# Optimization experiments

Measured on AMD Instinct MI355X. Metric: run time of the kernel, lower is better.

## Reference

```python
import jax, jax.numpy as jnp
import numpy as np

NUM_HEADS = 8
EPS = 1e-12  # torch F.normalize eps


def setup_inputs() -> dict:
    key = jax.random.key(0)
    k1, k2, k3 = jax.random.split(key, 3)
    B, N, C = 8, 4096, 768
    x = jax.random.normal(k1, (B, N, C), dtype=jnp.float32)
    Wqkv = jax.random.normal(k2, (C, 3 * C), dtype=jnp.float32) * 0.02
    temperature = jnp.ones((NUM_HEADS, 1, 1), dtype=jnp.float32)
    Wproj = jax.random.normal(k3, (C, C), dtype=jnp.float32) * 0.02
    bproj = jnp.zeros((C,), dtype=jnp.float32)
    return {"x": x, "Wqkv": Wqkv, "temperature": temperature,
            "Wproj": Wproj, "bproj": bproj}


def _l2norm(t):
    # torch F.normalize(dim=-1): x / max(||x||, eps)
    n = jnp.sqrt(jnp.sum(t * t, axis=-1, keepdims=True))
    return t / jnp.maximum(n, EPS)


def reference(x, Wqkv, temperature, Wproj, bproj):
    B, N, C = x.shape
    H = NUM_HEADS
    Ch = C // H
    qkv = (x @ Wqkv).reshape(B, N, 3, H, Ch)
    qkv = qkv.transpose(2, 0, 3, 1, 4)           # (3, B, H, N, Ch)
    q, k, v = qkv[0], qkv[1], qkv[2]
    # transpose(-2,-1): attend over channels -> (B, H, Ch, N)
    q = jnp.swapaxes(q, -2, -1)
    k = jnp.swapaxes(k, -2, -1)
    v = jnp.swapaxes(v, -2, -1)
    q = _l2norm(q)
    k = _l2norm(k)
    # (B, H, Ch, Ch) channel-attention scores, scaled by learned temperature
    attn = jnp.einsum('bhcn,bhdn->bhcd', q, k) * temperature
    attn = jax.nn.softmax(attn, axis=-1)
    out = jnp.einsum('bhcd,bhdn->bhcn', attn, v)  # (B, H, Ch, N)
    out = out.transpose(0, 3, 1, 2).reshape(B, N, C)
    return out @ Wproj + bproj
```

## Files before the change

kernel.cpp:

```cpp
#include <hip/hip_runtime.h>
#include <cstdint>
#include <cstddef>

typedef unsigned short u16;
typedef short bf16x8 __attribute__((ext_vector_type(8)));
typedef unsigned short u16x4 __attribute__((ext_vector_type(4)));
typedef unsigned short u16x8 __attribute__((ext_vector_type(8)));
typedef float f32x4 __attribute__((ext_vector_type(4)));

#define EPSN 1e-12f

__device__ __forceinline__ u16 f2bf(float f) {
  uint32_t u = __builtin_bit_cast(uint32_t, f);
  u += 0x7FFFu + ((u >> 16) & 1u);
  return (u16)(u >> 16);
}
__device__ __forceinline__ float bf2f(u16 h) {
  uint32_t u = ((uint32_t)h) << 16;
  return __builtin_bit_cast(float, u);
}

__device__ __forceinline__ void gll16(const u16* g, u16* l) {
  __builtin_amdgcn_global_load_lds(
      (const __attribute__((address_space(1))) void*)g,
      (__attribute__((address_space(3))) void*)l, 16, 0, 0);
}

__global__ __launch_bounds__(256)
void k_cvtT(const float* __restrict__ x, u16* __restrict__ Xh,
            u16* __restrict__ XhT) {
  __shared__ u16 tr[64][68];
  const int tid = threadIdx.x;
  const int t0 = blockIdx.x * 64, k0 = blockIdx.y * 64, b = blockIdx.z;
  const size_t base = ((size_t)b * 4096 + t0) * 768 + k0;
#pragma unroll
  for (int p = 0; p < 4; p++) {
    const int r = (tid >> 4) + p * 16;
    const int c = (tid & 15) * 4;
    f32x4 v = *(const f32x4*)(x + base + (size_t)r * 768 + c);
    u16x4 o;
#pragma unroll
    for (int e = 0; e < 4; e++) o[e] = f2bf(v[e]);
    *(u16x4*)(Xh + base + (size_t)r * 768 + c) = o;
    tr[c + 0][r] = o[0];
    tr[c + 1][r] = o[1];
    tr[c + 2][r] = o[2];
    tr[c + 3][r] = o[3];
  }
  __syncthreads();
  const size_t tbase = ((size_t)b * 768 + k0) * 4096 + t0;
#pragma unroll
  for (int p = 0; p < 4; p++) {
    const int kk = (tid >> 4) + p * 16;
    const int ts = (tid & 15) * 4;
    u16x4 o;
#pragma unroll
    for (int e = 0; e < 4; e++) o[e] = tr[kk][ts + e];
    *(u16x4*)(XhT + tbase + (size_t)kk * 4096 + ts) = o;
  }
}

__global__ __launch_bounds__(256)
void k_wt(const float* __restrict__ W, u16* __restrict__ Wt, u16* __restrict__ Wvh) {
  __shared__ float tile[32][33];
  const int j0 = blockIdx.x * 32;
  const int k0 = blockIdx.y * 32;
  const int tx = threadIdx.x & 31;
  const int ty = threadIdx.x >> 5;
#pragma unroll
  for (int r = 0; r < 4; r++) {
    float v = W[(size_t)(k0 + ty + r * 8) * 2304 + j0 + tx];
    tile[ty + r * 8][tx] = v;
    if (j0 >= 1536)
      Wvh[(size_t)(k0 + ty + r * 8) * 768 + (j0 - 1536) + tx] = f2bf(v);
  }
  __syncthreads();
  if (j0 < 1536) {
#pragma unroll
    for (int r = 0; r < 4; r++)
      Wt[(size_t)(j0 + ty + r * 8) * 768 + k0 + tx] = f2bf(tile[tx][ty + r * 8]);
  }
}

template <int OUTF32B, int TRI>
__global__ __launch_bounds__(256, 3)
void k_gemm(const u16* __restrict__ A, const u16* __restrict__ Btp,
            void* __restrict__ Cp, const float* __restrict__ bias,
            int K, int lda, int ldb, int ldc,
            long aZ, long bZ, long cZ, int zK, long kss) {
  const int gx = gridDim.x, gy = gridDim.y;
  int f = blockIdx.x + gx * (blockIdx.y + gy * blockIdx.z);
  const int total = gx * gy * gridDim.z;
  const int q = total >> 3, rr = total & 7;
  const int xcd = f & 7, kk0 = f >> 3;
  f = (xcd < rr ? xcd * (q + 1) : rr * (q + 1) + (xcd - rr) * q) + kk0;
  const int bx = f % gx;
  const int tmp = f / gx;
  const int by = tmp % gy;
  const int bz = tmp / gy;

  int m0, n0;
  if constexpr (TRI) {
    const int ty = (bx >= 20) ? 5 : (bx >= 18) ? 4 : (bx >= 15) ? 3
                 : (bx >= 11) ? 2 : (bx >= 6) ? 1 : 0;
    const int txi = ty + (bx - (ty * 6 - (ty * (ty - 1)) / 2));
    m0 = ty * 128;
    n0 = txi * 128;
  } else {
    m0 = by * 128;
    n0 = bx * 128;
  }
  const int z = bz;
  const int bb = z / zK, ss = z % zK;
  const u16* Az = A + (long)bb * aZ + (long)ss * kss;
  const u16* Btz = Btp + (long)bb * bZ + (long)ss * kss;

  __shared__ u16 As[3 * 128 * 32];
  __shared__ u16 Bs[3 * 128 * 32];
  const int tid = threadIdx.x;
  const int lane = tid & 63;
  const int wid = tid >> 6;
  const int wr = wid >> 1, wc = wid & 1;
  const int fm = lane & 15, kg = lane >> 4;

  const int lr = lane >> 2;
  const int gk = (lane & 3) ^ ((lane >> 3) & 3);
  const u16* gA = Az + (size_t)(m0 + wid * 32 + lr) * lda + gk * 8;
  const u16* gB = Btz + (size_t)(n0 + wid * 32 + lr) * ldb + gk * 8;
  const size_t a16 = (size_t)16 * lda, b16 = (size_t)16 * ldb;
  u16* lA = As + wid * 1024;
  u16* lB = Bs + wid * 1024;
  const int kq = (kg ^ ((fm >> 1) & 3)) * 8;

  auto STAGE = [&](int slot, int ko) {
    u16* la = lA + slot * 4096;
    u16* lb = lB + slot * 4096;
    gll16(gA + ko, la);
    gll16(gA + ko + a16, la + 512);
    gll16(gB + ko, lb);
    gll16(gB + ko + b16, lb + 512);
  };

  const int nt = K >> 5;
  STAGE(0, 0);
  STAGE(1, 32);
  int sC = 0, sN = 1, sS = 2;

  f32x4 acc[4][4] = {};
  for (int t = 0; t < nt; ++t) {
    if (t + 2 < nt) {
      STAGE(sS, (t + 2) * 32);
      __builtin_amdgcn_sched_barrier(0);
      asm volatile("s_waitcnt vmcnt(8)" ::: "memory");
    } else if (t + 2 == nt) {
      asm volatile("s_waitcnt vmcnt(4)" ::: "memory");
    } else {
      asm volatile("s_waitcnt vmcnt(0)" ::: "memory");
    }
    __builtin_amdgcn_sched_barrier(0);
    __builtin_amdgcn_s_barrier();
    __builtin_amdgcn_sched_barrier(0);

    const u16* as_ = As + sC * 4096;
    const u16* bs_ = Bs + sC * 4096;
    bf16x8 af[4], bfr[4];
#pragma unroll
    for (int i = 0; i < 4; i++)
      af[i] = *(const bf16x8*)&as_[(wr * 64 + i * 16 + fm) * 32 + kq];
#pragma unroll
    for (int j = 0; j < 4; j++)
      bfr[j] = *(const bf16x8*)&bs_[(wc * 64 + j * 16 + fm) * 32 + kq];
    asm volatile("s_waitcnt lgkmcnt(0)" ::: "memory");
    __builtin_amdgcn_sched_barrier(0);
    __builtin_amdgcn_s_barrier();
    __builtin_amdgcn_sched_barrier(0);

#pragma unroll
    for (int i = 0; i < 4; i++)
#pragma unroll
      for (int j = 0; j < 4; j++)
        acc[i][j] = __builtin_amdgcn_mfma_f32_16x16x32_bf16(af[i], bfr[j], acc[i][j], 0, 0, 0);

    const int t2 = sC; sC = sN; sN = sS; sS = t2;
  }

  if constexpr (OUTF32B) {
    float* C = (float*)Cp + (long)z * cZ;
#pragma unroll
    for (int j = 0; j < 4; j++) {
      const int col = n0 + wc * 64 + j * 16 + fm;
      const float bj = bias[col];
#pragma unroll
      for (int i = 0; i < 4; i++) {
        const int r0 = m0 + wr * 64 + i * 16 + kg * 4;
#pragma unroll
        for (int r = 0; r < 4; r++)
          C[(size_t)(r0 + r) * ldc + col] = acc[i][j][r] + bj;
      }
    }
  } else {
    const int rb = TRI ? 0 : m0;
    const int cb = TRI ? 0 : n0;
    const int ld = TRI ? 128 : ldc;
    u16* C = (u16*)Cp + (long)z * cZ + (TRI ? (long)bx * 16384 : 0L);
#pragma unroll
    for (int j = 0; j < 4; j++) {
      const int col = cb + wc * 64 + j * 16 + fm;
#pragma unroll
      for (int i = 0; i < 4; i++) {
        const int r0 = rb + wr * 64 + i * 16 + kg * 4;
#pragma unroll
        for (int r = 0; r < 4; r++)
          C[(size_t)(r0 + r) * ld + col] = f2bf(acc[i][j][r]);
      }
    }
  }
}

__global__ __launch_bounds__(256)
void k_red(const u16* __restrict__ P, u16* __restrict__ O) {
  const int b = blockIdx.y;
  const int ti = blockIdx.x / 6, tj = blockIdx.x % 6;
  const bool mirror = ti > tj;
  const int a = mirror ? tj : ti;
  const int c2 = mirror ? ti : tj;
  const int src = a * 6 - (a * (a - 1)) / 2 + (c2 - a);
  __shared__ u16 lt[128 * 128];
  const int tid = threadIdx.x;
  const int r = tid >> 1;
  const int ch = (tid & 1) * 64;
  float acc[64] = {};
  for (int s = 0; s < 4; s++) {
    const u16* p = P + ((size_t)(b * 4 + s) * 344064 + (size_t)src * 16384);
    __syncthreads();
#pragma unroll
    for (int it = 0; it < 8; it++) {
      const int idx = (tid + it * 256) * 8;
      *(u16x8*)&lt[idx] = *(const u16x8*)(p + idx);
    }
    __syncthreads();
    if (!mirror) {
#pragma unroll
      for (int e = 0; e < 64; e++) acc[e] += bf2f(lt[r * 128 + ch + e]);
    } else {
#pragma unroll
      for (int e = 0; e < 64; e++) acc[e] += bf2f(lt[(ch + e) * 128 + r]);
    }
  }
  u16* o = O + (size_t)b * 589824 + (size_t)(ti * 128 + r) * 768 + tj * 128 + ch;
#pragma unroll
  for (int v8 = 0; v8 < 8; v8++) {
    u16x8 w;
#pragma unroll
    for (int e = 0; e < 8; e++) w[e] = f2bf(acc[v8 * 8 + e]);
    *(u16x8*)(o + v8 * 8) = w;
  }
}

__global__ __launch_bounds__(256)
void k_score(const u16* __restrict__ Tm, const u16* __restrict__ Wt,
             const float* __restrict__ temperature, float* __restrict__ Aattn) {
  const int h = blockIdx.x, b = blockIdx.y;
  const int bh = b * 8 + h;
  __shared__ u16 As[96 * 32];
  __shared__ u16 Bs[96 * 32];
  __shared__ u16 Dt2[96 * 32];
  __shared__ u16 Dwq[96 * 32];
  __shared__ float Gs[96 * 96];
  __shared__ float nqs[96], nks[96], invk[96];

  const int tid = threadIdx.x;
  const int lane = tid & 63;
  const int wid = tid >> 6;
  const int wr = wid >> 1, wc = wid & 1;
  const int fm = lane & 15, kg = lane >> 4;
  const int lr = lane >> 2;
  const int gkS = (lane & 3) ^ ((lane >> 3) & 3);
  const int gkL = (lane & 3);
  const int kq = (kg ^ ((fm >> 1) & 3)) * 8;

  const u16* baseT1 = Tm + (size_t)b * 1179648 + (size_t)(h * 96) * 768;
  const u16* baseT2 = baseT1 + (size_t)768 * 768;
  const u16* baseWq = Wt + (size_t)(h * 96) * 768;
  const u16* baseWk = baseWq + (size_t)768 * 768;

  const u16* gsrc;
  u16* ldst;
  int gblk = gkS;
  if (wid == 0) { gsrc = baseT1; ldst = As; }
  else if (wid == 1) { gsrc = baseWk; ldst = Bs; }
  else if (wid == 2) { gsrc = baseT2; ldst = Dt2; gblk = gkL; }
  else { gsrc = baseWq; ldst = Dwq; gblk = gkL; }

  f32x4 acc[3][3] = {};
  float nqa = 0.f, nka = 0.f;
  const int sw1 = (tid < 96) ? ((tid >> 1) & 3) : 0;
  const int sw2 = (tid >= 128 && tid < 224) ? (((tid - 128) >> 1) & 3) : 0;

  for (int k0 = 0; k0 < 768; k0 += 32) {
    __syncthreads();
#pragma unroll
    for (int c = 0; c < 6; c++) {
      gll16(gsrc + (size_t)(c * 16 + lr) * 768 + k0 + gblk * 8,
            ldst + c * 512);
    }
    __syncthreads();
    bf16x8 af[3], bfr[3];
#pragma unroll
    for (int i = 0; i < 3; i++)
      af[i] = *(const bf16x8*)&As[(wr * 48 + i * 16 + fm) * 32 + kq];
#pragma unroll
    for (int j = 0; j < 3; j++)
      bfr[j] = *(const bf16x8*)&Bs[(wc * 48 + j * 16 + fm) * 32 + kq];
#pragma unroll
    for (int i = 0; i < 3; i++)
#pragma unroll
      for (int j = 0; j < 3; j++)
        acc[i][j] = __builtin_amdgcn_mfma_f32_16x16x32_bf16(af[i], bfr[j], acc[i][j], 0, 0, 0);
    if (tid < 96) {
#pragma unroll
      for (int g = 0; g < 4; g++) {
        u16x8 av = *(const u16x8*)&As[tid * 32 + (g ^ sw1) * 8];
        u16x8 w = *(const u16x8*)&Dwq[tid * 32 + g * 8];
#pragma unroll
        for (int e = 0; e < 8; e++) nqa += bf2f(av[e]) * bf2f(w[e]);
      }
    } else if (tid >= 128 && tid < 224) {
      const int d = tid - 128;
#pragma unroll
      for (int g = 0; g < 4; g++) {
        u16x8 av = *(const u16x8*)&Bs[d * 32 + (g ^ sw2) * 8];
        u16x8 w = *(const u16x8*)&Dt2[d * 32 + g * 8];
#pragma unroll
        for (int e = 0; e < 8; e++) nka += bf2f(av[e]) * bf2f(w[e]);
      }
    }
  }

  if (tid < 96) nqs[tid] = nqa;
  if (tid >= 128 && tid < 224) nks[tid - 128] = nka;
#pragma unroll
  for (int i = 0; i < 3; i++)
#pragma unroll
    for (int j = 0; j < 3; j++)
#pragma unroll
      for (int r = 0; r < 4; r++)
        Gs[(wr * 48 + i * 16 + kg * 4 + r) * 96 + wc * 48 + j * 16 + fm] = acc[i][j][r];
  __syncthreads();
  if (tid < 96) invk[tid] = 1.0f / fmaxf(sqrtf(nks[tid]), EPSN);
  __syncthreads();
  if (tid < 96) {
    const int c = tid;
    const float iq = temperature[h] / fmaxf(sqrtf(nqs[c]), EPSN);
    float sv[96];
    float m = -1e30f;
#pragma unroll
    for (int d = 0; d < 96; d++) {
      float s = Gs[c * 96 + d] * iq * invk[d];
      sv[d] = s;
      m = fmaxf(m, s);
    }
    float sum = 0.f;
#pragma unroll
    for (int d = 0; d < 96; d++) {
      float e = __expf(sv[d] - m);
      sv[d] = e;
      sum += e;
    }
    const float inv = 1.0f / sum;
    float* dst = Aattn + (size_t)bh * 9216 + (size_t)c * 96;
#pragma unroll
    for (int d = 0; d < 96; d++) dst[d] = sv[d] * inv;
  }
}

__global__ __launch_bounds__(256)
void k_weff(const float* __restrict__ Aattn, const float* __restrict__ Wproj,
            u16* __restrict__ Weff) {
  const int jt = blockIdx.x, h = blockIdx.y, b = blockIdx.z;
  const int bh = b * 8 + h;
  __shared__ float As2[9216];
  const int tid = threadIdx.x;
  for (int idx = tid; idx < 9216; idx += 256)
    As2[idx] = Aattn[(size_t)bh * 9216 + idx];
  __syncthreads();
  const int jloc = tid & 127;
  const int half = tid >> 7;
  const int j = jt * 128 + jloc;
  float acc[48] = {};
  for (int c = 0; c < 96; c++) {
    const float w = Wproj[(size_t)(h * 96 + c) * 768 + j];
    const f32x4* ar = (const f32x4*)&As2[c * 96 + half * 48];
#pragma unroll
    for (int v4 = 0; v4 < 12; v4++) {
      f32x4 av = ar[v4];
      acc[v4 * 4 + 0] += w * av[0];
      acc[v4 * 4 + 1] += w * av[1];
      acc[v4 * 4 + 2] += w * av[2];
      acc[v4 * 4 + 3] += w * av[3];
    }
  }
  u16* dst = Weff + ((size_t)b * 768 + j) * 768 + h * 96 + half * 48;
#pragma unroll
  for (int v4 = 0; v4 < 12; v4++) {
    u16x4 o;
    o[0] = f2bf(acc[v4 * 4 + 0]);
    o[1] = f2bf(acc[v4 * 4 + 1]);
    o[2] = f2bf(acc[v4 * 4 + 2]);
    o[3] = f2bf(acc[v4 * 4 + 3]);
    *(u16x4*)(dst + v4 * 4) = o;
  }
}

extern "C" void kernel_launch(void* const* d_in, const int* in_sizes, int n_in,
                              void* d_out, int out_size, void* d_ws, size_t ws_size,
                              hipStream_t stream) {
  const float* x = (const float*)d_in[0];
  const float* Wqkv = (const float*)d_in[1];
  const float* temp = (const float*)d_in[2];
  const float* Wproj = (const float*)d_in[3];
  const float* bproj = (const float*)d_in[4];
  float* out = (float*)d_out;

  char* ws = (char*)d_ws;
  u16* Xh = (u16*)ws;
  u16* XhT = (u16*)(ws + 50331648);
  u16* Wt = (u16*)(ws + 100663296);
  u16* Wvh = (u16*)(ws + 103022592);
  u16* XtXp = (u16*)(ws + 104202240);
  u16* XtXbf = (u16*)(ws + 141950976);
  u16* T = (u16*)(ws + 151388160);
  u16* WeffT = (u16*)(ws + 151388160);
  u16* WcompT = (u16*)(ws + 160825344);
  float* Aattn = (float*)(ws + 170262528);

  k_cvtT<<<dim3(64, 12, 8), 256, 0, stream>>>(x, Xh, XhT);
  k_wt<<<dim3(72, 24), 256, 0, stream>>>(Wqkv, Wt, Wvh);
  k_gemm<0, 1><<<dim3(21, 1, 32), 256, 0, stream>>>(
      XhT, XhT, (void*)XtXp, nullptr, 1024, 4096, 4096, 0,
      3145728L, 3145728L, 344064L, 4, 1024L);
  k_red<<<dim3(36, 8), 256, 0, stream>>>(XtXp, XtXbf);
  k_gemm<0, 0><<<dim3(6, 12, 8), 256, 0, stream>>>(
      Wt, XtXbf, (void*)T, nullptr, 768, 768, 768, 768,
      0L, 589824L, 1179648L, 1, 0L);
  k_score<<<dim3(8, 8), 256, 0, stream>>>(T, Wt, temp, Aattn);
  k_weff<<<dim3(6, 8, 8), 256, 0, stream>>>(Aattn, Wproj, WeffT);
  k_gemm<0, 0><<<dim3(6, 6, 8), 256, 0, stream>>>(
      WeffT, Wvh, (void*)WcompT, nullptr, 768, 768, 768, 768,
      589824L, 0L, 589824L, 1, 0L);
  k_gemm<1, 0><<<dim3(6, 32, 8), 256, 0, stream>>>(
      Xh, WcompT, out, bproj, 768, 768, 768, 768,
      3145728L, 589824L, 3145728L, 1, 0L);
}
```

Baseline: 297.2 us.

## Drop second GEMM barrier by staging after wait; vectorize transpose LDS writes

The GEMM main loop now issues the prefetch for slot t+2 after the per-iteration barrier instead of before it. That makes the second barrier, which protected slot reuse, unnecessary, so it is removed and each k-step has one barrier instead of two. The wait count becomes vmcnt(4) because only the next stage is outstanding at the wait. This shortens the prefetch distance, so load latency may be exposed. Separately, the convert/transpose kernel has each thread load a 4x4 block and write packed u16x4 rows to LDS, then read them back vectorized, replacing scalar 2-byte LDS accesses.

Measured after the change: 298.3 us. About the same (+0.4%).

```diff
diff --git a/kernel.cpp b/kernel.cpp
--- a/kernel.cpp
+++ b/kernel.cpp
@@ -32,20 +32,25 @@
   __shared__ u16 tr[64][68];
   const int tid = threadIdx.x;
   const int t0 = blockIdx.x * 64, k0 = blockIdx.y * 64, b = blockIdx.z;
+  const int rq = tid >> 4;
+  const int cq = tid & 15;
   const size_t base = ((size_t)b * 4096 + t0) * 768 + k0;
-#pragma unroll
-  for (int p = 0; p < 4; p++) {
-    const int r = (tid >> 4) + p * 16;
-    const int c = (tid & 15) * 4;
-    f32x4 v = *(const f32x4*)(x + base + (size_t)r * 768 + c);
+  u16 m[4][4];
+#pragma unroll
+  for (int e = 0; e < 4; e++) {
+    const int r = rq * 4 + e;
+    f32x4 v = *(const f32x4*)(x + base + (size_t)r * 768 + cq * 4);
     u16x4 o;
 #pragma unroll
-    for (int e = 0; e < 4; e++) o[e] = f2bf(v[e]);
-    *(u16x4*)(Xh + base + (size_t)r * 768 + c) = o;
-    tr[c + 0][r] = o[0];
-    tr[c + 1][r] = o[1];
-    tr[c + 2][r] = o[2];
-    tr[c + 3][r] = o[3];
+    for (int q = 0; q < 4; q++) o[q] = f2bf(v[q]);
+    *(u16x4*)(Xh + base + (size_t)r * 768 + cq * 4) = o;
+    m[e][0] = o[0]; m[e][1] = o[1]; m[e][2] = o[2]; m[e][3] = o[3];
+  }
+#pragma unroll
+  for (int q = 0; q < 4; q++) {
+    u16x4 w;
+    w[0] = m[0][q]; w[1] = m[1][q]; w[2] = m[2][q]; w[3] = m[3][q];
+    *(u16x4*)&tr[cq * 4 + q][rq * 4] = w;
   }
   __syncthreads();
   const size_t tbase = ((size_t)b * 768 + k0) * 4096 + t0;
@@ -53,9 +58,7 @@
   for (int p = 0; p < 4; p++) {
     const int kk = (tid >> 4) + p * 16;
     const int ts = (tid & 15) * 4;
-    u16x4 o;
-#pragma unroll
-    for (int e = 0; e < 4; e++) o[e] = tr[kk][ts + e];
+    u16x4 o = *(const u16x4*)&tr[kk][ts];
     *(u16x4*)(XhT + tbase + (size_t)kk * 4096 + ts) = o;
   }
 }
@@ -144,15 +147,11 @@
   const int nt = K >> 5;
   STAGE(0, 0);
   STAGE(1, 32);
-  int sC = 0, sN = 1, sS = 2;
+  int sl = 0;
 
   f32x4 acc[4][4] = {};
   for (int t = 0; t < nt; ++t) {
-    if (t + 2 < nt) {
-      STAGE(sS, (t + 2) * 32);
-      __builtin_amdgcn_sched_barrier(0);
-      asm volatile("s_waitcnt vmcnt(8)" ::: "memory");
-    } else if (t + 2 == nt) {
+    if (t + 1 < nt) {
       asm volatile("s_waitcnt vmcnt(4)" ::: "memory");
     } else {
       asm volatile("s_waitcnt vmcnt(0)" ::: "memory");
@@ -161,8 +160,13 @@
     __builtin_amdgcn_s_barrier();
     __builtin_amdgcn_sched_barrier(0);
 
-    const u16* as_ = As + sC * 4096;
-    const u16* bs_ = Bs + sC * 4096;
+    if (t + 2 < nt) {
+      int s2 = sl + 2; if (s2 >= 3) s2 -= 3;
+      STAGE(s2, (t + 2) * 32);
+    }
+
+    const u16* as_ = As + sl * 4096;
+    const u16* bs_ = Bs + sl * 4096;
     bf16x8 af[4], bfr[4];
 #pragma unroll
     for (int i = 0; i < 4; i++)
@@ -172,8 +176,6 @@
       bfr[j] = *(const bf16x8*)&bs_[(wc * 64 + j * 16 + fm) * 32 + kq];
     asm volatile("s_waitcnt lgkmcnt(0)" ::: "memory");
     __builtin_amdgcn_sched_barrier(0);
-    __builtin_amdgcn_s_barrier();
-    __builtin_amdgcn_sched_barrier(0);
 
 #pragma unroll
     for (int i = 0; i < 4; i++)
@@ -181,7 +183,7 @@
       for (int j = 0; j < 4; j++)
         acc[i][j] = __builtin_amdgcn_mfma_f32_16x16x32_bf16(af[i], bfr[j], acc[i][j], 0, 0, 0);
 
-    const int t2 = sC; sC = sN; sN = sS; sS = t2;
+    sl++; if (sl == 3) sl = 0;
   }
 
   if constexpr (OUTF32B) {
```
